# Optimization experiments

Measured on AMD Instinct MI355X. Metric: run time of the kernel, lower is better.

Reference implementation:

```python
import jax, jax.numpy as jnp
import numpy as np

EMBED = 768
FF = 3072
EPS = 1e-5


def _layernorm(x, gamma, beta):
    mu = jnp.mean(x, axis=-1, keepdims=True)
    var = jnp.var(x, axis=-1, keepdims=True)
    return (x - mu) * jax.lax.rsqrt(var + EPS) * gamma + beta


def setup_inputs() -> dict:
    key = jax.random.key(0)
    ks = jax.random.split(key, 12)
    s = EMBED ** -0.5
    inp = {
        "x": jax.random.normal(ks[0], (8, 1024, EMBED), dtype=jnp.float32),
        "Wq": jax.random.normal(ks[1], (EMBED, EMBED), dtype=jnp.float32) * s,
        "bq": jnp.zeros((EMBED,), jnp.float32),
        "Wk": jax.random.normal(ks[2], (EMBED, EMBED), dtype=jnp.float32) * s,
        "bk": jnp.zeros((EMBED,), jnp.float32),
        "Wv": jax.random.normal(ks[3], (EMBED, EMBED), dtype=jnp.float32) * s,
        "bv": jnp.zeros((EMBED,), jnp.float32),
        "W1": jax.random.normal(ks[4], (EMBED, FF), dtype=jnp.float32) * s,
        "b1": jnp.zeros((FF,), jnp.float32),
        "W2": jax.random.normal(ks[5], (FF, EMBED), dtype=jnp.float32) * (FF ** -0.5),
        "b2": jnp.zeros((EMBED,), jnp.float32),
        "g1": jnp.ones((EMBED,), jnp.float32),
        "beta1": jnp.zeros((EMBED,), jnp.float32),
        "g2": jnp.ones((EMBED,), jnp.float32),
        "beta2": jnp.zeros((EMBED,), jnp.float32),
    }
    return inp


def reference(x, Wq, bq, Wk, bk, Wv, bv, W1, b1, W2, b2, g1, beta1, g2, beta2):
    scale = x.shape[-1] ** -0.5
    # Single-head self-attention (no head split, faithful to source)
    Q = x @ Wq + bq  # [b, s, d]
    K = x @ Wk + bk
    V = x @ Wv + bv
    scores = jnp.einsum("bqd,bkd->bqk", Q, K) * scale
    attn = jax.nn.softmax(scores, axis=-1)
    attn_out = jnp.einsum("bqk,bkd->bqd", attn, V)
    x = x + _layernorm(attn_out, g1, beta1)
    # FFN (dropout is identity in eval mode); torch GELU default = exact erf
    h = jax.nn.gelu(x @ W1 + b1, approximate=False)
    ffn_out = h @ W2 + b2
    return x + _layernorm(ffn_out, g2, beta2)
```

## Files before the change

kernel.cpp:

```cpp
#include <hip/hip_runtime.h>
#include <cstdint>
#include <cstddef>

typedef __bf16 bf16;
typedef __bf16 bf16x8 __attribute__((ext_vector_type(8)));
typedef __bf16 bf16x4 __attribute__((ext_vector_type(4)));
typedef float  f32x4  __attribute__((ext_vector_type(4)));

#define EMBED 768
#define FF    3072
#define SEQ   1024
#define BATCH 8
#define ROWS  (BATCH * SEQ)

__global__ void cvt_bf16_kernel(const float* __restrict__ in, bf16* __restrict__ out,
                                float* __restrict__ rowsum, int n4) {
  int i = blockIdx.x * 256 + threadIdx.x;
  if (i < n4) {
    float4 v = ((const float4*)in)[i];
    bf16x4 o;
    o.x = (bf16)v.x; o.y = (bf16)v.y; o.z = (bf16)v.z; o.w = (bf16)v.w;
    ((bf16x4*)out)[i] = o;
  }
  if (i < ROWS) rowsum[i] = 0.f;
}

__global__ void transpose_bf16_kernel(const float* __restrict__ in, bf16* __restrict__ out,
                                      int K, int N) {
  __shared__ float tile[32][33];
  int nb = blockIdx.x * 32, kb = blockIdx.y * 32;
  for (int i = threadIdx.y; i < 32; i += 8)
    tile[i][threadIdx.x] = in[(size_t)(kb + i) * N + nb + threadIdx.x];
  __syncthreads();
  for (int i = threadIdx.y; i < 32; i += 8)
    out[(size_t)(nb + i) * K + kb + threadIdx.x] = (bf16)tile[threadIdx.x][i];
}

__global__ void transpose3_bf16_kernel(const float* __restrict__ w0, const float* __restrict__ w1,
                                       const float* __restrict__ w2, bf16* __restrict__ out) {
  __shared__ float tile[32][33];
  const float* in = (blockIdx.z == 0) ? w0 : (blockIdx.z == 1 ? w1 : w2);
  bf16* dst = out + (size_t)blockIdx.z * EMBED * EMBED;
  int nb = blockIdx.x * 32, kb = blockIdx.y * 32;
  for (int i = threadIdx.y; i < 32; i += 8)
    tile[i][threadIdx.x] = in[(size_t)(kb + i) * EMBED + nb + threadIdx.x];
  __syncthreads();
  for (int i = threadIdx.y; i < 32; i += 8)
    dst[(size_t)(nb + i) * EMBED + kb + threadIdx.x] = (bf16)tile[threadIdx.x][i];
}

enum { MODE_QKV = 0, MODE_EXP = 1, MODE_F32 = 2, MODE_GELU = 3, MODE_SPLIT = 4 };

template <int MODE>
__global__ void gemm_nt(const bf16* __restrict__ A, const bf16* __restrict__ B,
                        void* __restrict__ C, const float* __restrict__ bias, float alpha,
                        int M, int N, int K, int lda, int ldb, long sA, long sB, long sC,
                        void* __restrict__ C2, void* __restrict__ C3,
                        const float* __restrict__ bias2, const float* __restrict__ bias3) {
  __shared__ bf16 sAl[128 * 64];
  __shared__ bf16 sBl[128 * 64];
  const int tid  = threadIdx.x;
  const int lane = tid & 63;
  const int wave = tid >> 6;
  const int wm   = (wave >> 1) * 64;
  const int wn   = (wave & 1) * 64;
  const int quad = lane >> 4;
  const int l15  = lane & 15;
  const int l7   = lane & 7;

  int bx = blockIdx.x, by = blockIdx.y;
  if (gridDim.z == 1 && (gridDim.y & 7) == 0) {
    const int gx = gridDim.x, gy = gridDim.y;
    const int b  = by * gx + bx;
    const int xcd = b & 7, s = b >> 3;
    bx = s % gx;
    by = xcd * (gy >> 3) + s / gx;
  }

  int split = 0, batch = blockIdx.z;
  if constexpr (MODE == MODE_SPLIT) { split = blockIdx.z & 1; batch = blockIdx.z >> 1; }

  const bf16* Ab = A + (size_t)batch * sA + (size_t)split * K + (size_t)by * 128 * lda;
  const bf16* Bb = B + (size_t)batch * sB + (size_t)split * K + (size_t)bx * 128 * ldb;

  f32x4 acc[4][4] = {};

  for (int k0 = 0; k0 < K; k0 += 64) {
#pragma unroll
    for (int c = 0; c < 4; ++c) {
      int f   = c * 256 + tid;
      int row = f >> 3;
      int col = ((f & 7) ^ (row & 7)) * 8;
      __builtin_amdgcn_global_load_lds(
          (__attribute__((address_space(1))) void*)(Ab + (size_t)row * lda + k0 + col),
          (__attribute__((address_space(3))) void*)(sAl + (size_t)(c * 256 + wave * 64) * 8),
          16, 0, 0);
      __builtin_amdgcn_global_load_lds(
          (__attribute__((address_space(1))) void*)(Bb + (size_t)row * ldb + k0 + col),
          (__attribute__((address_space(3))) void*)(sBl + (size_t)(c * 256 + wave * 64) * 8),
          16, 0, 0);
    }
    __syncthreads();
#pragma unroll
    for (int kk = 0; kk < 2; ++kk) {
      const int ga = (((kk << 2) | quad) ^ l7) * 8;
      bf16x8 af[4], bfr[4];
#pragma unroll
      for (int t = 0; t < 4; ++t) {
        af[t]  = *(const bf16x8*)&sAl[(wm + t * 16 + l15) * 64 + ga];
        bfr[t] = *(const bf16x8*)&sBl[(wn + t * 16 + l15) * 64 + ga];
      }
#pragma unroll
      for (int mt = 0; mt < 4; ++mt)
#pragma unroll
        for (int nt = 0; nt < 4; ++nt)
          acc[mt][nt] = __builtin_amdgcn_mfma_f32_16x16x32_bf16(af[mt], bfr[nt], acc[mt][nt], 0, 0, 0);
    }
    __syncthreads();
  }

  const size_t mbase = (size_t)by * 128 + wm + quad * 4;

  if constexpr (MODE == MODE_QKV) {
    const int region = (bx * 128) / 768;
    const int nloc0  = bx * 128 - region * 768 + wn + l15;
    const float* bs  = (region == 0) ? bias : (region == 1 ? bias2 : bias3);
    const float  a   = (region == 0) ? alpha : 1.0f;
#pragma unroll
    for (int mt = 0; mt < 4; ++mt)
#pragma unroll
      for (int r = 0; r < 4; ++r) {
        size_t m = mbase + mt * 16 + r;
#pragma unroll
        for (int nt = 0; nt < 4; ++nt) {
          int nl  = nloc0 + nt * 16;
          float v = (acc[mt][nt][r] + bs[nl]) * a;
          if (region == 0)      ((bf16*)C )[m * EMBED + nl] = (bf16)v;
          else if (region == 1) ((bf16*)C2)[m * EMBED + nl] = (bf16)v;
          else {
            size_t b = m >> 10, s = m & 1023;
            ((bf16*)C3)[b * ((size_t)EMBED * SEQ) + (size_t)nl * SEQ + s] = (bf16)v;
          }
        }
      }
  } else if constexpr (MODE == MODE_EXP) {
    float* rowsum = (float*)C2;
#pragma unroll
    for (int mt = 0; mt < 4; ++mt)
#pragma unroll
      for (int r = 0; r < 4; ++r) {
        size_t m = mbase + mt * 16 + r;
        float part = 0.f;
#pragma unroll
        for (int nt = 0; nt < 4; ++nt) {
          size_t n = (size_t)bx * 128 + wn + l15 + nt * 16;
          float e = __expf(acc[mt][nt][r]);
          part += e;
          ((bf16*)C)[(size_t)batch * sC + m * N + n] = (bf16)e;
        }
        part += __shfl_xor(part, 1);
        part += __shfl_xor(part, 2);
        part += __shfl_xor(part, 4);
        part += __shfl_xor(part, 8);
        if (l15 == 0) atomicAdd(&rowsum[(size_t)batch * SEQ + m], part);
      }
  } else if constexpr (MODE == MODE_SPLIT) {
    bf16* Cp = (bf16*)(split ? C2 : C) + (size_t)batch * sC;
#pragma unroll
    for (int mt = 0; mt < 4; ++mt)
#pragma unroll
      for (int r = 0; r < 4; ++r) {
        size_t m = mbase + mt * 16 + r;
#pragma unroll
        for (int nt = 0; nt < 4; ++nt) {
          size_t n = (size_t)bx * 128 + wn + l15 + nt * 16;
          Cp[m * N + n] = (bf16)acc[mt][nt][r];
        }
      }
  } else {
    const size_t nbase = (size_t)bx * 128 + wn + l15;
#pragma unroll
    for (int mt = 0; mt < 4; ++mt)
#pragma unroll
      for (int r = 0; r < 4; ++r) {
        size_t m = mbase + mt * 16 + r;
#pragma unroll
        for (int nt = 0; nt < 4; ++nt) {
          size_t n = nbase + nt * 16;
          float v = acc[mt][nt][r];
          if (bias) v += bias[n];
          v *= alpha;
          if constexpr (MODE == MODE_GELU) {
            float y = 1.5957691216f * (v + 0.044715f * v * v * v);
            float g = v * __builtin_amdgcn_rcpf(1.0f + __expf(-y));
            ((bf16*)C)[m * (size_t)N + n] = (bf16)g;
          } else {
            ((float*)C)[(size_t)batch * sC + m * (size_t)N + n] = v;
          }
        }
      }
  }
}

template <int HAS_RS, int HAS_BIAS, int OUT_F32>
__global__ void add_ln_kernel(const bf16* __restrict__ xres, const bf16* __restrict__ y0,
                              const bf16* __restrict__ y1, const float* __restrict__ yb,
                              const float* __restrict__ rowsum,
                              const float* __restrict__ g, const float* __restrict__ beta,
                              float* __restrict__ out, bf16* __restrict__ outb) {
  const int lane = threadIdx.x & 63;
  const int wv   = threadIdx.x >> 6;
  const size_t row = (size_t)blockIdx.x * 4 + wv;
  const float inv_rs = HAS_RS ? (1.0f / rowsum[row]) : 1.0f;
  const bf16x4* y0p = (const bf16x4*)(y0 + row * EMBED);
  const bf16x4* y1p = (const bf16x4*)(y1 + row * EMBED);
  float v[12];
  float s = 0.f, q = 0.f;
#pragma unroll
  for (int c = 0; c < 3; ++c) {
    int ch = c * 64 + lane;
    bf16x4 a = y0p[ch], b = y1p[ch];
#pragma unroll
    for (int j = 0; j < 4; ++j) {
      float t = ((float)a[j] + (float)b[j]) * inv_rs;
      if (HAS_BIAS) t += yb[ch * 4 + j];
      v[c * 4 + j] = t; s += t; q += t * t;
    }
  }
#pragma unroll
  for (int o = 1; o < 64; o <<= 1) { s += __shfl_xor(s, o); q += __shfl_xor(q, o); }
  const float mu  = s * (1.0f / EMBED);
  const float var = q * (1.0f / EMBED) - mu * mu;
  const float inv = rsqrtf(var + 1e-5f);
  const bf16x4* xp = (const bf16x4*)(xres + row * EMBED);
#pragma unroll
  for (int c = 0; c < 3; ++c) {
    int ch = c * 64 + lane;
    bf16x4 xv = xp[ch];
    float4 o4; bf16x4 ob;
#pragma unroll
    for (int j = 0; j < 4; ++j) {
      int col = ch * 4 + j;
      float o = (v[c * 4 + j] - mu) * inv * g[col] + beta[col] + (float)xv[j];
      ((float*)&o4)[j] = o;
      ob[j] = (bf16)o;
    }
    if (OUT_F32) ((float4*)(out + row * EMBED))[ch] = o4;
    else         ((bf16x4*)(outb + row * EMBED))[ch] = ob;
  }
}

extern "C" void kernel_launch(void* const* d_in, const int* in_sizes, int n_in,
                              void* d_out, int out_size, void* d_ws, size_t ws_size,
                              hipStream_t stream) {
  const float* x   = (const float*)d_in[0];
  const float* Wq  = (const float*)d_in[1];
  const float* bq  = (const float*)d_in[2];
  const float* Wk  = (const float*)d_in[3];
  const float* bk  = (const float*)d_in[4];
  const float* Wv  = (const float*)d_in[5];
  const float* bv  = (const float*)d_in[6];
  const float* W1  = (const float*)d_in[7];
  const float* b1  = (const float*)d_in[8];
  const float* W2  = (const float*)d_in[9];
  const float* b2  = (const float*)d_in[10];
  const float* g1  = (const float*)d_in[11];
  const float* be1 = (const float*)d_in[12];
  const float* g2  = (const float*)d_in[13];
  const float* be2 = (const float*)d_in[14];

  char* ws = (char*)d_ws;
  bf16*  xb    = (bf16*)(ws + 0);
  bf16*  WqkvT = (bf16*)(ws + 12582912);
  bf16*  W1T   = (bf16*)(ws + 16121856);
  bf16*  W2T   = (bf16*)(ws + 20840448);
  bf16*  x1b   = (bf16*)(ws + 25559040);
  bf16*  Qs    = (bf16*)(ws + 38141952);
  bf16*  Kb    = (bf16*)(ws + 50724864);
  bf16*  VT    = (bf16*)(ws + 63307776);
  float* rowsum= (float*)(ws + 75890688);
  bf16*  P     = (bf16*)(ws + 92667904);
  bf16*  att0  = (bf16*)(ws + 109445120);
  bf16*  att1  = (bf16*)(ws + 134610944);
  bf16*  H     = (bf16*)(ws + 38141952);
  bf16*  F0    = (bf16*)(ws + 109445120);
  bf16*  F1    = (bf16*)(ws + 134610944);

  const float scale = 0.036084391824351615f;

  cvt_bf16_kernel<<<(ROWS * EMBED / 4) / 256, 256, 0, stream>>>(x, xb, rowsum, ROWS * EMBED / 4);
  dim3 tb(32, 8);
  transpose3_bf16_kernel<<<dim3(24, 24, 3), tb, 0, stream>>>(Wq, Wk, Wv, WqkvT);
  transpose_bf16_kernel<<<dim3(FF / 32, EMBED / 32), tb, 0, stream>>>(W1, W1T, EMBED, FF);
  transpose_bf16_kernel<<<dim3(EMBED / 32, FF / 32), tb, 0, stream>>>(W2, W2T, FF, EMBED);

  gemm_nt<MODE_QKV><<<dim3(2304 / 128, ROWS / 128, 1), 256, 0, stream>>>(
      xb, WqkvT, Qs, bq, scale, ROWS, 2304, EMBED, EMBED, EMBED, 0, 0, 0, Kb, VT, bk, bv);

  gemm_nt<MODE_EXP><<<dim3(SEQ / 128, SEQ / 128, BATCH), 256, 0, stream>>>(
      Qs, Kb, P, nullptr, 1.f, SEQ, SEQ, EMBED, EMBED, EMBED,
      (long)SEQ * EMBED, (long)SEQ * EMBED, (long)SEQ * SEQ,
      rowsum, nullptr, nullptr, nullptr);

  gemm_nt<MODE_SPLIT><<<dim3(EMBED / 128, SEQ / 128, BATCH * 2), 256, 0, stream>>>(
      P, VT, att0, nullptr, 1.f, SEQ, EMBED, SEQ / 2, SEQ, SEQ,
      (long)SEQ * SEQ, (long)EMBED * SEQ, (long)SEQ * EMBED, att1, nullptr, nullptr, nullptr);

  add_ln_kernel<1, 0, 0><<<ROWS / 4, 256, 0, stream>>>(
      xb, att0, att1, nullptr, rowsum, g1, be1, nullptr, x1b);

  gemm_nt<MODE_GELU><<<dim3(FF / 128, ROWS / 128, 1), 256, 0, stream>>>(
      x1b, W1T, H, b1, 1.f, ROWS, FF, EMBED, EMBED, EMBED, 0, 0, 0,
      nullptr, nullptr, nullptr, nullptr);

  gemm_nt<MODE_SPLIT><<<dim3(EMBED / 128, ROWS / 128, 2), 256, 0, stream>>>(
      H, W2T, F0, nullptr, 1.f, ROWS, EMBED, FF / 2, FF, FF, 0, 0, 0,
      F1, nullptr, nullptr, nullptr);

  add_ln_kernel<0, 1, 1><<<ROWS / 4, 256, 0, stream>>>(
      x1b, F0, F1, b2, nullptr, g2, be2, (float*)d_out, nullptr);
}
```

Measured before the change: 371.2 us.

## Double-buffer GEMM LDS tiles with K=32 stages and vectorize V-transpose stores

Rewrites the gemm_nt main loop to split K into 32-wide stages held in two LDS buffers. The next stage's global-to-LDS loads are issued before computing the current one, so memory latency overlaps MFMA work and each iteration needs one barrier instead of two, at the cost of a new XOR swizzle and smaller per-stage work. It also changes the QKV epilogue for the transposed V region to pack four consecutive sequence elements into one bf16x4 store instead of scattered scalar stores.

```diff
diff --git a/kernel.cpp b/kernel.cpp
--- a/kernel.cpp
+++ b/kernel.cpp
@@ -57,8 +57,8 @@
                         int M, int N, int K, int lda, int ldb, long sA, long sB, long sC,
                         void* __restrict__ C2, void* __restrict__ C3,
                         const float* __restrict__ bias2, const float* __restrict__ bias3) {
-  __shared__ bf16 sAl[128 * 64];
-  __shared__ bf16 sBl[128 * 64];
+  __shared__ bf16 sAl[2][128 * 32];
+  __shared__ bf16 sBl[2][128 * 32];
   const int tid  = threadIdx.x;
   const int lane = tid & 63;
   const int wave = tid >> 6;
@@ -66,7 +66,6 @@
   const int wn   = (wave & 1) * 64;
   const int quad = lane >> 4;
   const int l15  = lane & 15;
-  const int l7   = lane & 7;
 
   int bx = blockIdx.x, by = blockIdx.y;
   if (gridDim.z == 1 && (gridDim.y & 7) == 0) {
@@ -83,39 +82,46 @@
   const bf16* Ab = A + (size_t)batch * sA + (size_t)split * K + (size_t)by * 128 * lda;
   const bf16* Bb = B + (size_t)batch * sB + (size_t)split * K + (size_t)bx * 128 * ldb;
 
-  f32x4 acc[4][4] = {};
-
-  for (int k0 = 0; k0 < K; k0 += 64) {
-#pragma unroll
-    for (int c = 0; c < 4; ++c) {
-      int f   = c * 256 + tid;
-      int row = f >> 3;
-      int col = ((f & 7) ^ (row & 7)) * 8;
+  auto issue = [&](int k0, int buf) {
+#pragma unroll
+    for (int c = 0; c < 2; ++c) {
+      int f    = c * 256 + tid;
+      int row  = f >> 2;
+      int slot = f & 3;
+      int col  = (slot ^ ((row >> 1) & 3)) * 8;
       __builtin_amdgcn_global_load_lds(
           (__attribute__((address_space(1))) void*)(Ab + (size_t)row * lda + k0 + col),
-          (__attribute__((address_space(3))) void*)(sAl + (size_t)(c * 256 + wave * 64) * 8),
+          (__attribute__((address_space(3))) void*)(sAl[buf] + (size_t)(c * 256 + wave * 64) * 8),
           16, 0, 0);
       __builtin_amdgcn_global_load_lds(
           (__attribute__((address_space(1))) void*)(Bb + (size_t)row * ldb + k0 + col),
-          (__attribute__((address_space(3))) void*)(sBl + (size_t)(c * 256 + wave * 64) * 8),
+          (__attribute__((address_space(3))) void*)(sBl[buf] + (size_t)(c * 256 + wave * 64) * 8),
           16, 0, 0);
     }
-    __syncthreads();
-#pragma unroll
-    for (int kk = 0; kk < 2; ++kk) {
-      const int ga = (((kk << 2) | quad) ^ l7) * 8;
-      bf16x8 af[4], bfr[4];
-#pragma unroll
-      for (int t = 0; t < 4; ++t) {
-        af[t]  = *(const bf16x8*)&sAl[(wm + t * 16 + l15) * 64 + ga];
-        bfr[t] = *(const bf16x8*)&sBl[(wn + t * 16 + l15) * 64 + ga];
-      }
-#pragma unroll
-      for (int mt = 0; mt < 4; ++mt)
-#pragma unroll
-        for (int nt = 0; nt < 4; ++nt)
-          acc[mt][nt] = __builtin_amdgcn_mfma_f32_16x16x32_bf16(af[mt], bfr[nt], acc[mt][nt], 0, 0, 0);
-    }
+  };
+
+  f32x4 acc[4][4] = {};
+
+  const int nst = K >> 5;
+  issue(0, 0);
+  __syncthreads();
+  for (int i = 0; i < nst; ++i) {
+    if (i + 1 < nst) issue((i + 1) << 5, (i + 1) & 1);
+    const bf16* sa = sAl[i & 1];
+    const bf16* sb = sBl[i & 1];
+    bf16x8 af[4], bfr[4];
+#pragma unroll
+    for (int t = 0; t < 4; ++t) {
+      const int ra = wm + t * 16 + l15;
+      const int rb = wn + t * 16 + l15;
+      af[t]  = *(const bf16x8*)&sa[ra * 32 + (quad ^ ((ra >> 1) & 3)) * 8];
+      bfr[t] = *(const bf16x8*)&sb[rb * 32 + (quad ^ ((rb >> 1) & 3)) * 8];
+    }
+#pragma unroll
+    for (int mt = 0; mt < 4; ++mt)
+#pragma unroll
+      for (int nt = 0; nt < 4; ++nt)
+        acc[mt][nt] = __builtin_amdgcn_mfma_f32_16x16x32_bf16(af[mt], bfr[nt], acc[mt][nt], 0, 0, 0);
     __syncthreads();
   }
 
@@ -126,23 +132,34 @@
     const int nloc0  = bx * 128 - region * 768 + wn + l15;
     const float* bs  = (region == 0) ? bias : (region == 1 ? bias2 : bias3);
     const float  a   = (region == 0) ? alpha : 1.0f;
-#pragma unroll
-    for (int mt = 0; mt < 4; ++mt)
-#pragma unroll
-      for (int r = 0; r < 4; ++r) {
-        size_t m = mbase + mt * 16 + r;
+    if (region == 2) {
+#pragma unroll
+      for (int mt = 0; mt < 4; ++mt)
 #pragma unroll
         for (int nt = 0; nt < 4; ++nt) {
-          int nl  = nloc0 + nt * 16;
-          float v = (acc[mt][nt][r] + bs[nl]) * a;
-          if (region == 0)      ((bf16*)C )[m * EMBED + nl] = (bf16)v;
-          else if (region == 1) ((bf16*)C2)[m * EMBED + nl] = (bf16)v;
-          else {
-            size_t b = m >> 10, s = m & 1023;
-            ((bf16*)C3)[b * ((size_t)EMBED * SEQ) + (size_t)nl * SEQ + s] = (bf16)v;
+          size_t m0 = mbase + mt * 16;
+          int nl = nloc0 + nt * 16;
+          bf16x4 pk;
+#pragma unroll
+          for (int r = 0; r < 4; ++r) pk[r] = (bf16)(acc[mt][nt][r] + bs[nl]);
+          size_t b = m0 >> 10, s = m0 & 1023;
+          *(bf16x4*)&((bf16*)C3)[b * ((size_t)EMBED * SEQ) + (size_t)nl * SEQ + s] = pk;
+        }
+    } else {
+#pragma unroll
+      for (int mt = 0; mt < 4; ++mt)
+#pragma unroll
+        for (int r = 0; r < 4; ++r) {
+          size_t m = mbase + mt * 16 + r;
+#pragma unroll
+          for (int nt = 0; nt < 4; ++nt) {
+            int nl  = nloc0 + nt * 16;
+            float v = (acc[mt][nt][r] + bs[nl]) * a;
+            if (region == 0) ((bf16*)C )[m * EMBED + nl] = (bf16)v;
+            else             ((bf16*)C2)[m * EMBED + nl] = (bf16)v;
           }
         }
-      }
+    }
   } else if constexpr (MODE == MODE_EXP) {
     float* rowsum = (float*)C2;
 #pragma unroll
```

New measurement: 382.5 us. 1.03x slower.
